# Kernel optimization log

Hardware: AMD Instinct MI355X
Metric: run time of the kernel (lower is better)

Reference implementation:

```python
import jax, jax.numpy as jnp
import numpy as np
import math

N_HEAD = 12

def _tiled_causal_mask(T):
    # t x t lower-triangular mask tiled 3x3 -> T x T (T divisible by 3)
    t = T // 3
    tril = jnp.tril(jnp.ones((t, t), dtype=bool))
    return jnp.tile(tril, (3, 3))  # [T, T]

def setup_inputs() -> dict:
    key = jax.random.key(0)
    ks = jax.random.split(key, 5)
    B, T, C = 4, 1536, 768
    s = 1.0 / math.sqrt(C)
    return {
        "x": jax.random.normal(ks[0], (B, T, C), dtype=jnp.float32),
        "Wq": jax.random.normal(ks[1], (C, C), dtype=jnp.float32) * s,
        "bq": jnp.zeros((C,), dtype=jnp.float32),
        "Wk": jax.random.normal(ks[2], (C, C), dtype=jnp.float32) * s,
        "bk": jnp.zeros((C,), dtype=jnp.float32),
        "Wv": jax.random.normal(ks[3], (C, C), dtype=jnp.float32) * s,
        "bv": jnp.zeros((C,), dtype=jnp.float32),
        "Wp": jax.random.normal(ks[4], (C, C), dtype=jnp.float32) * s,
        "bp": jnp.zeros((C,), dtype=jnp.float32),
    }

def reference(x, Wq, bq, Wk, bk, Wv, bv, Wp, bp):
    B, T, C = x.shape
    H = N_HEAD
    D = C // H  # head dim
    def heads(W, b):
        return (x @ W.T + b).reshape(B, T, H, D).transpose(0, 2, 1, 3)  # [B,H,T,D]
    q = heads(Wq, bq)
    k = heads(Wk, bk)
    v = heads(Wv, bv)
    att = jnp.einsum('bhqd,bhkd->bhqk', q, k) * (1.0 / math.sqrt(D))  # [B,H,T,T]
    mask = _tiled_causal_mask(T)  # [T,T] bool
    att = jnp.where(mask[None, None], att, jnp.float32(-jnp.inf))
    att = jax.nn.softmax(att, axis=-1)
    y = jnp.einsum('bhqk,bhkd->bhqd', att, v)  # [B,H,T,D]
    y = y.transpose(0, 2, 1, 3).reshape(B, T, C)
    return y @ Wp.T + bp
```

## Files before the change

### kernel.cpp

```cpp
#include <hip/hip_runtime.h>
#include <hip/hip_bf16.h>

typedef __attribute__((ext_vector_type(8))) short bf16x8;
typedef __attribute__((ext_vector_type(4))) float f32x4;

#define NH 12
#define HD 64
#define TT 1536
#define CC 768
#define BB 4
#define MM (BB * TT)
#define LOG2E 1.44269504088896f
#define SSHIFT 14.4269504089f

__device__ __forceinline__ unsigned short f2bf(float f) {
    unsigned int u = __builtin_bit_cast(unsigned int, f);
    return (unsigned short)((u + 0x7FFFu + ((u >> 16) & 1u)) >> 16);
}

__device__ __forceinline__ unsigned short nbf(float f) {
    __hip_bfloat16 h = __float2bfloat16(f);
    return __builtin_bit_cast(unsigned short, h);
}

__device__ __forceinline__ void gl_lds16(const unsigned short* g, unsigned short* l) {
    __builtin_amdgcn_global_load_lds(
        (const __attribute__((address_space(1))) void*)g,
        (__attribute__((address_space(3))) void*)l,
        16, 0, 0);
}

#define N4W (CC * CC / 4)
#define N4X (MM * CC / 4)
__global__ __launch_bounds__(256) void convert_all(
    const float* __restrict__ x,
    const float* __restrict__ w0, const float* __restrict__ w1,
    const float* __restrict__ w2, const float* __restrict__ w3,
    unsigned short* __restrict__ xo,
    unsigned short* __restrict__ o0, unsigned short* __restrict__ o1,
    unsigned short* __restrict__ o2, unsigned short* __restrict__ o3) {
    int i = blockIdx.x * 256 + threadIdx.x;
    const float* in;
    unsigned short* out;
    int j;
    if (i < N4X) {
        in = x; out = xo; j = i;
    } else {
        int t = i - N4X;
        int which = t / N4W;
        j = t - which * N4W;
        in = which == 0 ? w0 : which == 1 ? w1 : which == 2 ? w2 : w3;
        out = which == 0 ? o0 : which == 1 ? o1 : which == 2 ? o2 : o3;
    }
    float4 v = reinterpret_cast<const float4*>(in)[j];
    ushort4 o = { f2bf(v.x), f2bf(v.y), f2bf(v.z), f2bf(v.w) };
    reinterpret_cast<ushort4*>(out)[j] = o;
}

#define GEMM_KLOOP(APTR, BPTR, APASS, MI)                                     \
    for (int kt = 0; kt < 12; kt++) {                                         \
        const int k0 = kt * 64;                                               \
        __syncthreads();                                                      \
        _Pragma("unroll")                                                     \
        for (int i = 0; i < APASS; i++)                                       \
            gl_lds16(&APTR[(size_t)(m0 + i * 32 + sr) * CC + k0 + sc],        \
                     as0 + (i * 32 + w * 8) * 64);                            \
        _Pragma("unroll")                                                     \
        for (int i = 0; i < 4; i++)                                           \
            gl_lds16(&BPTR[(size_t)(n0 + i * 32 + sr) * CC + k0 + sc],        \
                     bs0 + (i * 32 + w * 8) * 64);                            \
        __syncthreads();                                                      \
        _Pragma("unroll")                                                     \
        for (int s = 0; s < 2; s++) {                                         \
            const int swz = ((s * 4 + fg) ^ (fr & 7)) * 8;                    \
            bf16x8 a[MI], b[4];                                               \
            _Pragma("unroll")                                                 \
            for (int mi = 0; mi < MI; mi++)                                   \
                a[mi] = *reinterpret_cast<const bf16x8*>(                     \
                    as0 + (wr * (MI * 16) + mi * 16 + fr) * 64 + swz);        \
            _Pragma("unroll")                                                 \
            for (int ni = 0; ni < 4; ni++)                                    \
                b[ni] = *reinterpret_cast<const bf16x8*>(                     \
                    bs0 + (wc * 64 + ni * 16 + fr) * 64 + swz);               \
            _Pragma("unroll")                                                 \
            for (int mi = 0; mi < MI; mi++)                                   \
                _Pragma("unroll")                                             \
                for (int ni = 0; ni < 4; ni++)                                \
                    acc[mi][ni] = __builtin_amdgcn_mfma_f32_16x16x32_bf16(    \
                        a[mi], b[ni], acc[mi][ni], 0, 0, 0);                  \
        }                                                                     \
    }

__global__ __launch_bounds__(256) void gemm_qkv(
    const unsigned short* __restrict__ xb,
    const unsigned short* __restrict__ wq, const float* __restrict__ bq,
    const unsigned short* __restrict__ wk, const float* __restrict__ bk,
    const unsigned short* __restrict__ wv, const float* __restrict__ bv,
    unsigned short* __restrict__ qo, unsigned short* __restrict__ ko,
    unsigned short* __restrict__ vo) {
    __shared__ unsigned short As[64][64];
    __shared__ unsigned short Bs[128][64];

    const int wg = (blockIdx.x & 7) * 216 + (blockIdx.x >> 3);
    const int z = wg / 576;
    const int rem = wg % 576;
    const int m0 = (rem / 6) * 64;
    const int n0 = (rem % 6) * 128;

    const unsigned short* W = (z == 0) ? wq : (z == 1) ? wk : wv;
    const float* bias = (z == 0) ? bq : (z == 1) ? bk : bv;
    unsigned short* out = (z == 0) ? qo : (z == 1) ? ko : vo;
    const float scale = (z == 0) ? 0.125f * LOG2E : 1.0f;

    const int tid = threadIdx.x;
    const int lane = tid & 63;
    const int w = tid >> 6;
    const int wr = w >> 1, wc = w & 1;
    const int fr = lane & 15, fg = lane >> 4;

    const int sr = tid >> 3;
    const int sc = ((tid & 7) ^ ((tid >> 3) & 7)) * 8;
    unsigned short* as0 = &As[0][0];
    unsigned short* bs0 = &Bs[0][0];

    f32x4 acc[2][4];
#pragma unroll
    for (int ni = 0; ni < 4; ni++) {
        float bv_ = bias[n0 + wc * 64 + ni * 16 + fr];
#pragma unroll
        for (int mi = 0; mi < 2; mi++)
            acc[mi][ni] = (f32x4){bv_, bv_, bv_, bv_};
    }

    GEMM_KLOOP(xb, W, 2, 2)

#pragma unroll
    for (int mi = 0; mi < 2; mi++)
#pragma unroll
        for (int ni = 0; ni < 4; ni++) {
            int n = n0 + wc * 64 + ni * 16 + fr;
            int h = n >> 6, d = n & 63;
            int m_base = m0 + wr * 32 + mi * 16 + fg * 4;
            int b_ = m_base / TT, t0 = m_base % TT;
            if (z == 2) {
                size_t off = ((size_t)(b_ * NH + h) * HD + d) * (size_t)TT + t0;
                ushort4 o = { nbf(acc[mi][ni][0]), nbf(acc[mi][ni][1]),
                              nbf(acc[mi][ni][2]), nbf(acc[mi][ni][3]) };
                *reinterpret_cast<ushort4*>(&out[off]) = o;
            } else {
#pragma unroll
                for (int r = 0; r < 4; r++) {
                    size_t off = ((size_t)(b_ * NH + h) * TT + t0 + r) * (size_t)HD + d;
                    out[off] = nbf(acc[mi][ni][r] * scale);
                }
            }
        }
}

__global__ __launch_bounds__(256) void gemm_proj(
    const unsigned short* __restrict__ yb,
    const unsigned short* __restrict__ wp, const float* __restrict__ bp,
    float* __restrict__ out) {
    __shared__ unsigned short As[64][64];
    __shared__ unsigned short Bs[128][64];

    const int wg = (blockIdx.x & 7) * 72 + (blockIdx.x >> 3);
    const int m0 = (wg / 6) * 64;
    const int n0 = (wg % 6) * 128;

    const int tid = threadIdx.x;
    const int lane = tid & 63;
    const int w = tid >> 6;
    const int wr = w >> 1, wc = w & 1;
    const int fr = lane & 15, fg = lane >> 4;

    const int sr = tid >> 3;
    const int sc = ((tid & 7) ^ ((tid >> 3) & 7)) * 8;
    unsigned short* as0 = &As[0][0];
    unsigned short* bs0 = &Bs[0][0];

    f32x4 acc[2][4];
#pragma unroll
    for (int ni = 0; ni < 4; ni++) {
        float bv_ = bp[n0 + wc * 64 + ni * 16 + fr];
#pragma unroll
        for (int mi = 0; mi < 2; mi++)
            acc[mi][ni] = (f32x4){bv_, bv_, bv_, bv_};
    }

    GEMM_KLOOP(yb, wp, 2, 2)

#pragma unroll
    for (int mi = 0; mi < 2; mi++)
#pragma unroll
        for (int ni = 0; ni < 4; ni++) {
            int n = n0 + wc * 64 + ni * 16 + fr;
#pragma unroll
            for (int r = 0; r < 4; r++) {
                int m = m0 + wr * 32 + mi * 16 + fg * 4 + r;
                out[(size_t)m * CC + n] = acc[mi][ni][r];
            }
        }
}

__global__ __launch_bounds__(256) void attn(
    const unsigned short* __restrict__ q, const unsigned short* __restrict__ k,
    const unsigned short* __restrict__ vt, unsigned short* __restrict__ y) {
    __shared__ unsigned short Ks[2][32][72];
    __shared__ unsigned short Vs[2][64][40];
    __shared__ unsigned short Ps[4][16][40];

    const int gid = blockIdx.x;
    const int slot = gid & 7;
    const int sub = (gid >> 3) % 6;
    const int bh = slot * 6 + sub;
    const int qt = gid / 48;
    const int qseg = 7 - qt / 3;
    const int sg0 = qt % 3;
    const int q0 = sg0 * 512 + qseg * 64;

    const int tid = threadIdx.x;
    const int w = tid >> 6;
    const int lane = tid & 63;
    const int fr = lane & 15, fg = lane >> 4;

    const size_t base = (size_t)bh * TT * HD;

    bf16x8 aq[2];
#pragma unroll
    for (int s = 0; s < 2; s++)
        aq[s] = *reinterpret_cast<const bf16x8*>(
            &q[base + (size_t)(q0 + w * 16 + fr) * HD + s * 32 + fg * 8]);

    f32x4 acc_o[4];
#pragma unroll
    for (int i = 0; i < 4; i++) acc_o[i] = (f32x4){0.f, 0.f, 0.f, 0.f};
    f32x4 acc_l = (f32x4){0.f, 0.f, 0.f, 0.f};

    const bf16x8 ones8 = {(short)0x3F80, (short)0x3F80, (short)0x3F80, (short)0x3F80,
                          (short)0x3F80, (short)0x3F80, (short)0x3F80, (short)0x3F80};
    const f32x4 sinit = {-SSHIFT, -SSHIFT, -SSHIFT, -SSHIFT};

    const int kr = tid >> 3, kc = tid & 7;
    const int vr = tid >> 2, vc = tid & 3;

    uint4 kreg, vreg;
    auto issue = [&](int k0n) {
        kreg = *reinterpret_cast<const uint4*>(&k[base + (size_t)(k0n + kr) * HD + kc * 8]);
        vreg = *reinterpret_cast<const uint4*>(&vt[base + (size_t)vr * TT + k0n + vc * 8]);
    };
    auto wlds = [&](int b) {
        *reinterpret_cast<uint4*>(&Ks[b][kr][kc * 8]) = kreg;
        *reinterpret_cast<uint4*>(&Vs[b][vr][vc * 8]) = vreg;
    };

    const int per = 2 * qseg + 2;
    const int ntot = 3 * per;

    issue(0);
    wlds(0);
    int cur = 0;
    int j = 0;
    int ji = 0, si = 0;

    for (int ci = 0; ci < ntot; ci++) {
        if (ci + 1 < ntot) {
            ji++; if (ji == per) { ji = 0; si++; }
            issue(si * 512 + ji * 32);
        }
        __syncthreads();

        f32x4 S[2];
#pragma unroll
        for (int nb = 0; nb < 2; nb++) {
            f32x4 sa = sinit;
#pragma unroll
            for (int s = 0; s < 2; s++) {
                bf16x8 bk_ = *reinterpret_cast<const bf16x8*>(
                    &Ks[cur][nb * 16 + fr][s * 32 + fg * 8]);
                sa = __builtin_amdgcn_mfma_f32_16x16x32_bf16(bk_, aq[s], sa, 0, 0, 0);
            }
            S[nb] = sa;
        }

        if (j >= 2 * qseg) {
            const int joff = (j - 2 * qseg) * 32;
            const int ib = w * 16 + fr;
#pragma unroll
            for (int nb = 0; nb < 2; nb++)
#pragma unroll
                for (int r = 0; r < 4; r++) {
                    int jb = joff + nb * 16 + fg * 4 + r;
                    if (jb > ib) S[nb][r] = -1e30f;
                }
        }

#pragma unroll
        for (int nb = 0; nb < 2; nb++) {
            unsigned int u0 = (unsigned int)nbf(exp2f(S[nb][0])) |
                              ((unsigned int)nbf(exp2f(S[nb][1])) << 16);
            unsigned int u1 = (unsigned int)nbf(exp2f(S[nb][2])) |
                              ((unsigned int)nbf(exp2f(S[nb][3])) << 16);
            *reinterpret_cast<uint2*>(&Ps[w][fr][nb * 16 + fg * 4]) = (uint2){u0, u1};
        }

        bf16x8 ap = *reinterpret_cast<const bf16x8*>(&Ps[w][fr][fg * 8]);
#pragma unroll
        for (int nd = 0; nd < 4; nd++) {
            bf16x8 bv_ = *reinterpret_cast<const bf16x8*>(&Vs[cur][nd * 16 + fr][fg * 8]);
            acc_o[nd] = __builtin_amdgcn_mfma_f32_16x16x32_bf16(ap, bv_, acc_o[nd], 0, 0, 0);
        }
        acc_l = __builtin_amdgcn_mfma_f32_16x16x32_bf16(ap, ones8, acc_l, 0, 0, 0);

        if (ci + 1 < ntot) wlds(cur ^ 1);
        cur ^= 1;
        if (++j == per) j = 0;
    }

    const int b_ = bh / NH, h = bh % NH;
#pragma unroll
    for (int r = 0; r < 4; r++) {
        float inv = 1.f / acc_l[r];
        int t = q0 + w * 16 + fg * 4 + r;
        size_t off = ((size_t)b_ * TT + t) * CC + h * HD;
#pragma unroll
        for (int nd = 0; nd < 4; nd++)
            y[off + nd * 16 + fr] = nbf(acc_o[nd][r] * inv);
    }
}

extern "C" void kernel_launch(void* const* d_in, const int* in_sizes, int n_in,
                              void* d_out, int out_size, void* d_ws, size_t ws_size,
                              hipStream_t stream) {
    const float* x  = (const float*)d_in[0];
    const float* Wq = (const float*)d_in[1];
    const float* bq = (const float*)d_in[2];
    const float* Wk = (const float*)d_in[3];
    const float* bk = (const float*)d_in[4];
    const float* Wv = (const float*)d_in[5];
    const float* bv = (const float*)d_in[6];
    const float* Wp = (const float*)d_in[7];
    const float* bp = (const float*)d_in[8];
    float* out = (float*)d_out;

    unsigned short* ws  = (unsigned short*)d_ws;
    unsigned short* wqb = ws;
    unsigned short* wkb = wqb + (size_t)CC * CC;
    unsigned short* wvb = wkb + (size_t)CC * CC;
    unsigned short* wpb = wvb + (size_t)CC * CC;
    unsigned short* xb  = wpb + (size_t)CC * CC;
    unsigned short* qb_ = xb  + (size_t)MM * CC;
    unsigned short* kb_ = qb_ + (size_t)MM * CC;
    unsigned short* vt_ = kb_ + (size_t)MM * CC;
    unsigned short* yb  = vt_ + (size_t)MM * CC;

    const int ntot4 = N4X + 4 * N4W;
    convert_all<<<(ntot4 + 255) / 256, 256, 0, stream>>>(
        x, Wq, Wk, Wv, Wp, xb, wqb, wkb, wvb, wpb);

    gemm_qkv<<<dim3(1728), 256, 0, stream>>>(
        xb, wqb, bq, wkb, bk, wvb, bv, qb_, kb_, vt_);
    attn<<<dim3(48 * 24), 256, 0, stream>>>(qb_, kb_, vt_, yb);
    gemm_proj<<<dim3(576), 256, 0, stream>>>(yb, wpb, bp, out);
}
```

Measured before the change: 97.39 us.

## Double attention query tile to 128 rows with 512-thread blocks

Each attention block now processes 128 query rows with 8 waves instead of 64 rows with 4 waves, which halves the grid to 576 blocks. Every K/V tile loaded into shared memory is reused by twice as many waves, cutting global loads and per-block overhead. K and V loading is split so half the threads fetch K and half fetch V, one 16-byte load each. The cost is fewer blocks for load balancing across the causal work distribution, and coarser masking granularity that may waste some compute on masked tiles.

Measured after the change: 104.3 us. 1.07x slower.

```diff
diff --git a/kernel.cpp b/kernel.cpp
--- a/kernel.cpp
+++ b/kernel.cpp
@@ -203,21 +203,21 @@
         }
 }
 
-__global__ __launch_bounds__(256) void attn(
+__global__ __launch_bounds__(512) void attn(
     const unsigned short* __restrict__ q, const unsigned short* __restrict__ k,
     const unsigned short* __restrict__ vt, unsigned short* __restrict__ y) {
     __shared__ unsigned short Ks[2][32][72];
     __shared__ unsigned short Vs[2][64][40];
-    __shared__ unsigned short Ps[4][16][40];
+    __shared__ unsigned short Ps[8][16][40];
 
     const int gid = blockIdx.x;
     const int slot = gid & 7;
-    const int sub = (gid >> 3) % 6;
-    const int bh = slot * 6 + sub;
-    const int qt = gid / 48;
-    const int qseg = 7 - qt / 3;
-    const int sg0 = qt % 3;
-    const int q0 = sg0 * 512 + qseg * 64;
+    const int rest = gid >> 3;
+    const int bh = slot * 6 + rest % 6;
+    const int rank = rest / 6;
+    const int p = 3 - rank / 3;
+    const int sg0 = rank % 3;
+    const int q0 = sg0 * 512 + p * 128;
 
     const int tid = threadIdx.x;
     const int w = tid >> 6;
@@ -241,20 +241,23 @@
                           (short)0x3F80, (short)0x3F80, (short)0x3F80, (short)0x3F80};
     const f32x4 sinit = {-SSHIFT, -SSHIFT, -SSHIFT, -SSHIFT};
 
-    const int kr = tid >> 3, kc = tid & 7;
-    const int vr = tid >> 2, vc = tid & 3;
-
-    uint4 kreg, vreg;
+    const bool isK = tid < 256;
+    const int t2 = tid & 255;
+    const int kr = t2 >> 3, kc = t2 & 7;
+    const int vr = t2 >> 2, vc = t2 & 3;
+
+    uint4 reg;
     auto issue = [&](int k0n) {
-        kreg = *reinterpret_cast<const uint4*>(&k[base + (size_t)(k0n + kr) * HD + kc * 8]);
-        vreg = *reinterpret_cast<const uint4*>(&vt[base + (size_t)vr * TT + k0n + vc * 8]);
+        reg = isK
+            ? *reinterpret_cast<const uint4*>(&k[base + (size_t)(k0n + kr) * HD + kc * 8])
+            : *reinterpret_cast<const uint4*>(&vt[base + (size_t)vr * TT + k0n + vc * 8]);
     };
     auto wlds = [&](int b) {
-        *reinterpret_cast<uint4*>(&Ks[b][kr][kc * 8]) = kreg;
-        *reinterpret_cast<uint4*>(&Vs[b][vr][vc * 8]) = vreg;
+        if (isK) *reinterpret_cast<uint4*>(&Ks[b][kr][kc * 8]) = reg;
+        else     *reinterpret_cast<uint4*>(&Vs[b][vr][vc * 8]) = reg;
     };
 
-    const int per = 2 * qseg + 2;
+    const int per = 4 * p + 4;
     const int ntot = 3 * per;
 
     issue(0);
@@ -283,8 +286,8 @@
             S[nb] = sa;
         }
 
-        if (j >= 2 * qseg) {
-            const int joff = (j - 2 * qseg) * 32;
+        if (j >= 4 * p) {
+            const int joff = (j - 4 * p) * 32;
             const int ib = w * 16 + fr;
 #pragma unroll
             for (int nb = 0; nb < 2; nb++)
@@ -360,6 +363,6 @@
 
     gemm_qkv<<<dim3(1728), 256, 0, stream>>>(
         xb, wqb, bq, wkb, bk, wvb, bv, qb_, kb_, vt_);
-    attn<<<dim3(48 * 24), 256, 0, stream>>>(qb_, kb_, vt_, yb);
+    attn<<<dim3(576), 512, 0, stream>>>(qb_, kb_, vt_, yb);
     gemm_proj<<<dim3(576), 256, 0, stream>>>(yb, wpb, bp, out);
 }
```
